# Optimization experiments

Hardware: AMD Instinct MI355X
Metric: run time of the kernel (lower is better)

## Reference

```python
import jax, jax.numpy as jnp
import numpy as np

EMB_DIM = 128
WEIGHT_COL = 24

def setup_inputs() -> dict:
    key = jax.random.key(0)
    ks = jax.random.split(key, 9)
    B, S = 8, 4096
    s_in = 1.0 / np.sqrt(EMB_DIM)
    s_out = 1.0 / np.sqrt(WEIGHT_COL)
    return {
        "x": jax.random.normal(ks[0], (B, S, EMB_DIM), dtype=jnp.float32),
        "wQ": jax.random.uniform(ks[1], (EMB_DIM, WEIGHT_COL), jnp.float32, -s_in, s_in),
        "bQ": jax.random.uniform(ks[2], (WEIGHT_COL,), jnp.float32, -s_in, s_in),
        "wK": jax.random.uniform(ks[3], (EMB_DIM, WEIGHT_COL), jnp.float32, -s_in, s_in),
        "bK": jax.random.uniform(ks[4], (WEIGHT_COL,), jnp.float32, -s_in, s_in),
        "wV": jax.random.uniform(ks[5], (EMB_DIM, WEIGHT_COL), jnp.float32, -s_in, s_in),
        "bV": jax.random.uniform(ks[6], (WEIGHT_COL,), jnp.float32, -s_in, s_in),
        "wO": jax.random.uniform(ks[7], (WEIGHT_COL, EMB_DIM), jnp.float32, -s_out, s_out),
        "bO": jax.random.uniform(ks[8], (EMB_DIM,), jnp.float32, -s_out, s_out),
    }

def reference(x, wQ, bQ, wK, bK, wV, bV, wO, bO):
    # projections: [B,S,E] -> [B,S,D]
    Q = x @ wQ + bQ
    K = x @ wK + bK
    V = x @ wV + bV
    # NOTE: source scales by sqrt(emb_dim), not sqrt(weight_col)
    scale = 1.0 / np.sqrt(EMB_DIM).astype(np.float32)
    scores = jnp.einsum('bqd,bkd->bqk', Q, K) * scale  # [B,S,S]
    A = jax.nn.softmax(scores, axis=-1)
    H = jnp.einsum('bqk,bkd->bqd', A, V)               # [B,S,D]
    return H @ wO + bO                                  # [B,S,E]
```

## Files before the change

kernel.cpp:

```cpp
#include <hip/hip_runtime.h>
#include <hip/hip_fp16.h>


#define B_ 8
#define S_ 4096
#define E_ 128
#define D_ 24
#define N_ (B_ * S_)
#define SCALE 0.08838834764831845f
#define LOG2E 1.4426950408889634f

#define NSP 8
#define KCHUNK (S_ / NSP)
#define TK 128

#define KS_STRIDE 40
#define VS_STRIDE 136
#define HS_STRIDE 40
#define XS_STRIDE 136
#define OS_STRIDE 84

typedef __attribute__((ext_vector_type(8))) short bfrag;
typedef __attribute__((ext_vector_type(4))) float ffrag;

__device__ inline unsigned short f2bf(float f) {
    unsigned int x = __builtin_bit_cast(unsigned int, f);
    return (unsigned short)((x + 0x7fffu + ((x >> 16) & 1u)) >> 16);
}
__device__ inline unsigned int pack2h(float a, float b) {
    unsigned int ua = __builtin_bit_cast(unsigned int, a) + 0x8000u;
    unsigned int ub = __builtin_bit_cast(unsigned int, b) + 0x8000u;
    return __builtin_amdgcn_perm(ub, ua, 0x07060302);
}
__device__ inline unsigned int packh16(float a, float b) {
    return __builtin_bit_cast(unsigned int, __builtin_amdgcn_cvt_pkrtz(a, b));
}

__global__ __launch_bounds__(256) void prep_kernel(
    const float* __restrict__ wQ, const float* __restrict__ bQ,
    const float* __restrict__ wK, const float* __restrict__ bK,
    const float* __restrict__ wV, const float* __restrict__ bV,
    const float* __restrict__ wO,
    unsigned short* __restrict__ Wf, unsigned short* __restrict__ wOf,
    float* __restrict__ bqkv)
{
    const int gtid   = blockIdx.x * 256 + threadIdx.x;
    const int stride = gridDim.x * 256;
    const float qs = SCALE * LOG2E;
    for (int idx = gtid; idx < 4 * 5 * 512; idx += stride) {
        const int j    = idx & 7;
        const int lane = (idx >> 3) & 63;
        const int nt   = (idx >> 9) % 5;
        const int kt   = idx / 2560;
        const int n = nt * 16 + (lane & 15);
        const int k = kt * 32 + ((lane >> 4) << 3) + j;
        float v = 0.0f;
        if (n < 24)      v = wQ[k * 24 + n] * qs;
        else if (n < 48) v = wK[k * 24 + (n - 24)];
        else if (n < 72) v = wV[k * 24 + (n - 48)];
        Wf[idx] = f2bf(v);
    }
    for (int idx = gtid; idx < 8 * 512; idx += stride) {
        const int j    = idx & 7;
        const int lane = (idx >> 3) & 63;
        const int nt   = idx >> 9;
        const int k = ((lane >> 4) << 3) + j;
        const int e = nt * 16 + (lane & 15);
        wOf[idx] = (k < 24) ? f2bf(wO[k * 128 + e]) : (unsigned short)0;
    }
    if (gtid < 80) {
        float v = 0.0f;
        if (gtid < 24)      v = bQ[gtid] * qs;
        else if (gtid < 48) v = bK[gtid - 24];
        else if (gtid < 72) v = bV[gtid - 48];
        bqkv[gtid] = v;
    }
}

__global__ __launch_bounds__(256) void proj_kernel(
    const float* __restrict__ x, const unsigned short* __restrict__ Wf,
    const float* __restrict__ bqkv,
    unsigned short* __restrict__ Qbf, unsigned short* __restrict__ Kbf,
    unsigned short* __restrict__ Vt)
{
    __shared__ float smem[64 * OS_STRIDE];
    unsigned short* xs = (unsigned short*)smem;
    float* os = smem;

    const int tid  = threadIdx.x;
    const int lane = tid & 63;
    const int w    = tid >> 6;
    const int col  = lane & 15;
    const int quad = lane >> 4;
    const int rb   = blockIdx.x * 64;

    #pragma unroll
    for (int i = 0; i < 8; ++i) {
        const int idx = i * 256 + tid;
        const int row = idx >> 5, c4 = idx & 31;
        const float4 xv = *(const float4*)(x + (size_t)(rb + row) * 128 + c4 * 4);
        uint2 h;
        h.x = pack2h(xv.x, xv.y);
        h.y = pack2h(xv.z, xv.w);
        *(uint2*)(&xs[row * XS_STRIDE + c4 * 4]) = h;
    }

    bfrag Wfr[20];
    #pragma unroll
    for (int f = 0; f < 20; ++f)
        Wfr[f] = *(const bfrag*)(Wf + (f * 64 + lane) * 8);

    __syncthreads();

    ffrag acc[5];
    #pragma unroll
    for (int nt = 0; nt < 5; ++nt) acc[nt] = (ffrag){0.f, 0.f, 0.f, 0.f};

    #pragma unroll
    for (int kt = 0; kt < 4; ++kt) {
        const bfrag Af = *(const bfrag*)(&xs[(w * 16 + col) * XS_STRIDE + kt * 32 + quad * 8]);
        #pragma unroll
        for (int nt = 0; nt < 5; ++nt)
            acc[nt] = __builtin_amdgcn_mfma_f32_16x16x32_bf16(Af, Wfr[kt * 5 + nt], acc[nt], 0, 0, 0);
    }

    __syncthreads();

    #pragma unroll
    for (int nt = 0; nt < 5; ++nt) {
        const float bb = bqkv[nt * 16 + col];
        #pragma unroll
        for (int r = 0; r < 4; ++r)
            os[(w * 16 + quad * 4 + r) * OS_STRIDE + nt * 16 + col] = acc[nt][r] + bb;
    }
    __syncthreads();

    {
        const int half  = tid & 1;
        const int row   = (tid >> 1) & 63;
        const int isK   = tid >> 7;
        const int cbase = isK * 24;
        unsigned int pk[8];
        #pragma unroll
        for (int g = 0; g < 8; ++g) {
            const int c0 = half * 16 + g * 2;
            const float f0 = (c0     < 24) ? os[row * OS_STRIDE + cbase + c0]     : 0.0f;
            const float f1 = (c0 + 1 < 24) ? os[row * OS_STRIDE + cbase + c0 + 1] : 0.0f;
            pk[g] = pack2h(f0, f1);
        }
        unsigned short* dst = (isK ? Kbf : Qbf) + (size_t)(rb + row) * 32 + half * 16;
        *(uint4*)(dst)     = make_uint4(pk[0], pk[1], pk[2], pk[3]);
        *(uint4*)(dst + 8) = make_uint4(pk[4], pk[5], pk[6], pk[7]);
    }

    if (tid < 192) {
        const int d  = tid % 24;
        const int ch = tid / 24;
        unsigned int p[4];
        #pragma unroll
        for (int g = 0; g < 4; ++g) {
            const float f0 = os[(ch * 8 + g * 2 + 0) * OS_STRIDE + 48 + d];
            const float f1 = os[(ch * 8 + g * 2 + 1) * OS_STRIDE + 48 + d];
            p[g] = pack2h(f0, f1);
        }
        const int b = rb >> 12, s0 = rb & 4095;
        uint4* dst = (uint4*)(Vt + (((size_t)(b * 32 + d)) << 12) + s0 + ch * 8);
        *dst = make_uint4(p[0], p[1], p[2], p[3]);
    } else if (tid < 200) {
        const int ch = tid - 192;
        const int b = rb >> 12, s0 = rb & 4095;
        uint4* dst = (uint4*)(Vt + (((size_t)(b * 32 + 24)) << 12) + s0 + ch * 8);
        *dst = make_uint4(0x3F803F80u, 0x3F803F80u, 0x3F803F80u, 0x3F803F80u);
    }
}

__global__ __launch_bounds__(256, 8) void attn_kernel(
    const unsigned short* __restrict__ Qbf, const unsigned short* __restrict__ Kbf,
    const unsigned short* __restrict__ Vt,
    __half* __restrict__ Opart, float* __restrict__ lpart)
{
    __shared__ unsigned short Ks[TK * KS_STRIDE];
    __shared__ unsigned short Vs[25 * VS_STRIDE];

    const int tid   = threadIdx.x;
    const int lane  = tid & 63;
    const int w     = tid >> 6;
    const int col   = lane & 15;
    const int quad  = lane >> 4;
    const int blk   = blockIdx.x;
    const int split = blockIdx.y;
    const int b     = blk >> 5;
    const int qbase = blk * 128 + w * 32;

    const bfrag Qf0 = *(const bfrag*)(Qbf + (size_t)(qbase + col) * 32 + quad * 8);
    const bfrag Qf1 = *(const bfrag*)(Qbf + (size_t)(qbase + 16 + col) * 32 + quad * 8);

    const unsigned short* Kbase = Kbf + ((size_t)b * 4096 + split * KCHUNK) * 32;
    const unsigned short* Vbase = Vt + (size_t)(b * 32) * 4096 + split * KCHUNK;

    const int r1 = (16 + col <= 24) ? (16 + col) : 24;

    ffrag O00 = {0.f,0.f,0.f,0.f};
    ffrag O01 = {0.f,0.f,0.f,0.f};
    ffrag O10 = {0.f,0.f,0.f,0.f};
    ffrag O11 = {0.f,0.f,0.f,0.f};

    for (int kb = 0; kb < KCHUNK; kb += TK) {
        #pragma unroll
        for (int i = 0; i < 2; ++i) {
            const int idx = i * 256 + tid;
            const int key = idx >> 2, ch = idx & 3;
            const uint4 t4 = *(const uint4*)(Kbase + (size_t)(kb + key) * 32 + ch * 8);
            const int row = (key & ~31) + (((key >> 2) & 1) << 4)
                          + (((key & 31) >> 3) << 2) + (key & 3);
            *(uint4*)(&Ks[row * KS_STRIDE + ch * 8]) = t4;
        }
        #pragma unroll
        for (int i = 0; i < 2; ++i) {
            const int idx = i * 256 + tid;
            if (idx < 400) {
                const int d = idx >> 4, ch = idx & 15;
                const uint4 t4 = *(const uint4*)(Vbase + (size_t)d * 4096 + kb + ch * 8);
                *(uint4*)(&Vs[d * VS_STRIDE + ch * 8]) = t4;
            }
        }
        __syncthreads();

        #pragma unroll
        for (int c2 = 0; c2 < 4; ++c2) {
            const bfrag Kfe = *(const bfrag*)(&Ks[(c2 * 32 + col) * KS_STRIDE + quad * 8]);
            const bfrag Kfo = *(const bfrag*)(&Ks[(c2 * 32 + 16 + col) * KS_STRIDE + quad * 8]);
            const bfrag Va0 = *(const bfrag*)(&Vs[col * VS_STRIDE + c2 * 32 + quad * 8]);
            const bfrag Va1 = *(const bfrag*)(&Vs[r1 * VS_STRIDE + c2 * 32 + quad * 8]);

            {
                ffrag Se = {0.f,0.f,0.f,0.f}, So = {0.f,0.f,0.f,0.f};
                Se = __builtin_amdgcn_mfma_f32_16x16x32_bf16(Kfe, Qf0, Se, 0, 0, 0);
                So = __builtin_amdgcn_mfma_f32_16x16x32_bf16(Kfo, Qf0, So, 0, 0, 0);
                union { bfrag f; unsigned int u[4]; } P;
                P.u[0] = pack2h(__builtin_amdgcn_exp2f(Se[0]), __builtin_amdgcn_exp2f(Se[1]));
                P.u[1] = pack2h(__builtin_amdgcn_exp2f(Se[2]), __builtin_amdgcn_exp2f(Se[3]));
                P.u[2] = pack2h(__builtin_amdgcn_exp2f(So[0]), __builtin_amdgcn_exp2f(So[1]));
                P.u[3] = pack2h(__builtin_amdgcn_exp2f(So[2]), __builtin_amdgcn_exp2f(So[3]));
                O00 = __builtin_amdgcn_mfma_f32_16x16x32_bf16(Va0, P.f, O00, 0, 0, 0);
                O01 = __builtin_amdgcn_mfma_f32_16x16x32_bf16(Va1, P.f, O01, 0, 0, 0);
            }
            {
                ffrag Se = {0.f,0.f,0.f,0.f}, So = {0.f,0.f,0.f,0.f};
                Se = __builtin_amdgcn_mfma_f32_16x16x32_bf16(Kfe, Qf1, Se, 0, 0, 0);
                So = __builtin_amdgcn_mfma_f32_16x16x32_bf16(Kfo, Qf1, So, 0, 0, 0);
                union { bfrag f; unsigned int u[4]; } P;
                P.u[0] = pack2h(__builtin_amdgcn_exp2f(Se[0]), __builtin_amdgcn_exp2f(Se[1]));
                P.u[1] = pack2h(__builtin_amdgcn_exp2f(Se[2]), __builtin_amdgcn_exp2f(Se[3]));
                P.u[2] = pack2h(__builtin_amdgcn_exp2f(So[0]), __builtin_amdgcn_exp2f(So[1]));
                P.u[3] = pack2h(__builtin_amdgcn_exp2f(So[2]), __builtin_amdgcn_exp2f(So[3]));
                O10 = __builtin_amdgcn_mfma_f32_16x16x32_bf16(Va0, P.f, O10, 0, 0, 0);
                O11 = __builtin_amdgcn_mfma_f32_16x16x32_bf16(Va1, P.f, O11, 0, 0, 0);
            }
        }
        __syncthreads();
    }

    {
        const size_t base0 = ((size_t)split * N_ + qbase + col) * 32;
        uint2 s0;
        s0.x = packh16(O00[0], O00[1]);
        s0.y = packh16(O00[2], O00[3]);
        *(uint2*)(Opart + base0 + quad * 4) = s0;
        if (quad < 2) {
            uint2 s1;
            s1.x = packh16(O01[0], O01[1]);
            s1.y = packh16(O01[2], O01[3]);
            *(uint2*)(Opart + base0 + 16 + quad * 4) = s1;
        }
        if (quad == 2)
            lpart[(size_t)split * N_ + qbase + col] = O01[0];

        const size_t base1 = base0 + 16 * 32;
        uint2 t0;
        t0.x = packh16(O10[0], O10[1]);
        t0.y = packh16(O10[2], O10[3]);
        *(uint2*)(Opart + base1 + quad * 4) = t0;
        if (quad < 2) {
            uint2 t1;
            t1.x = packh16(O11[0], O11[1]);
            t1.y = packh16(O11[2], O11[3]);
            *(uint2*)(Opart + base1 + 16 + quad * 4) = t1;
        }
        if (quad == 2)
            lpart[(size_t)split * N_ + qbase + 16 + col] = O11[0];
    }
}

__global__ __launch_bounds__(256) void combine_kernel(
    const __half* __restrict__ Opart, const float* __restrict__ lpart,
    const unsigned short* __restrict__ wOf, const float* __restrict__ bO,
    float* __restrict__ out)
{
    __shared__ unsigned short Hs[64 * HS_STRIDE];

    const int tid = threadIdx.x;
    const int qb  = blockIdx.x * 64;
    {
        const int ql = tid >> 2;
        const int c8 = (tid & 3) * 8;
        const int q  = qb + ql;
        float a[8] = {0.f, 0.f, 0.f, 0.f, 0.f, 0.f, 0.f, 0.f};
        if (c8 < 24) {
            #pragma unroll
            for (int s = 0; s < NSP; ++s) {
                const __half2* p2 = (const __half2*)(Opart + ((size_t)s * N_ + q) * 32 + c8);
                #pragma unroll
                for (int j = 0; j < 4; ++j) {
                    const float2 f = __half22float2(p2[j]);
                    a[2 * j]     += f.x;
                    a[2 * j + 1] += f.y;
                }
            }
        }
        float ls = 0.f;
        #pragma unroll
        for (int s = 0; s < NSP; ++s) ls += lpart[(size_t)s * N_ + q];
        const float inv = 1.0f / ls;
        uint4 pk;
        pk.x = pack2h(a[0] * inv, a[1] * inv);
        pk.y = pack2h(a[2] * inv, a[3] * inv);
        pk.z = pack2h(a[4] * inv, a[5] * inv);
        pk.w = pack2h(a[6] * inv, a[7] * inv);
        *(uint4*)(&Hs[ql * HS_STRIDE + c8]) = pk;
    }
    __syncthreads();

    const int lane = tid & 63;
    const int w    = tid >> 6;
    const int col  = lane & 15;
    const int quad = lane >> 4;
    const bfrag Hf = *(const bfrag*)(&Hs[(w * 16 + col) * HS_STRIDE + quad * 8]);
    #pragma unroll
    for (int nt = 0; nt < 8; ++nt) {
        const bfrag Wo = *(const bfrag*)(wOf + (nt * 64 + lane) * 8);
        ffrag C = {0.f, 0.f, 0.f, 0.f};
        C = __builtin_amdgcn_mfma_f32_16x16x32_bf16(Hf, Wo, C, 0, 0, 0);
        const float bo = bO[nt * 16 + col];
        #pragma unroll
        for (int r = 0; r < 4; ++r)
            out[(size_t)(qb + w * 16 + quad * 4 + r) * 128 + nt * 16 + col] = C[r] + bo;
    }
}

extern "C" void kernel_launch(void* const* d_in, const int* in_sizes, int n_in,
                              void* d_out, int out_size, void* d_ws, size_t ws_size,
                              hipStream_t stream) {
    const float* x  = (const float*)d_in[0];
    const float* wQ = (const float*)d_in[1];
    const float* bQ = (const float*)d_in[2];
    const float* wK = (const float*)d_in[3];
    const float* bK = (const float*)d_in[4];
    const float* wV = (const float*)d_in[5];
    const float* bV = (const float*)d_in[6];
    const float* wO = (const float*)d_in[7];
    const float* bO = (const float*)d_in[8];
    float* out = (float*)d_out;

    unsigned short* ws16 = (unsigned short*)d_ws;
    unsigned short* Qbf = ws16;
    unsigned short* Kbf = Qbf + (size_t)N_ * 32;
    unsigned short* Vt  = Kbf + (size_t)N_ * 32;
    unsigned short* Wf  = Vt + (size_t)B_ * 32 * S_;
    unsigned short* wOf = Wf + 4 * 5 * 512;
    float* bqkv = (float*)(wOf + 8 * 512);
    __half* Opart = (__half*)(bqkv + 80);
    float* lpart = (float*)(Opart + (size_t)NSP * N_ * 32);

    prep_kernel<<<8, 256, 0, stream>>>(wQ, bQ, wK, bK, wV, bV, wO, Wf, wOf, bqkv);
    proj_kernel<<<N_ / 64, 256, 0, stream>>>(x, Wf, bqkv, Qbf, Kbf, Vt);
    attn_kernel<<<dim3(N_ / 128, NSP), 256, 0, stream>>>(Qbf, Kbf, Vt, Opart, lpart);
    combine_kernel<<<N_ / 64, 256, 0, stream>>>(Opart, lpart, wOf, bO, out);
}
```

Measured before the change: 125.4 us.

## Double-buffer K/V tiles with register prefetch and larger attention blocks

The attention kernel now prefetches the next K/V tile from global memory into registers while it computes on the current tile from a double-buffered shared memory region. This removes one barrier per iteration and hides global load latency. Blocks grow to 512 threads covering 256 queries, and the key-split count drops from 8 to 4. That halves the partial outputs the combine kernel has to read, but leaves fewer blocks and longer per-block loops, and the larger LDS footprint lowers occupancy.

```diff
diff --git a/kernel.cpp b/kernel.cpp
--- a/kernel.cpp
+++ b/kernel.cpp
@@ -10,9 +10,10 @@
 #define SCALE 0.08838834764831845f
 #define LOG2E 1.4426950408889634f
 
-#define NSP 8
+#define NSP 4
 #define KCHUNK (S_ / NSP)
 #define TK 128
+#define NT (KCHUNK / TK)
 
 #define KS_STRIDE 40
 #define VS_STRIDE 136
@@ -174,13 +175,13 @@
     }
 }
 
-__global__ __launch_bounds__(256, 8) void attn_kernel(
+__global__ __launch_bounds__(512, 4) void attn_kernel(
     const unsigned short* __restrict__ Qbf, const unsigned short* __restrict__ Kbf,
     const unsigned short* __restrict__ Vt,
     __half* __restrict__ Opart, float* __restrict__ lpart)
 {
-    __shared__ unsigned short Ks[TK * KS_STRIDE];
-    __shared__ unsigned short Vs[25 * VS_STRIDE];
+    __shared__ unsigned short Ks[2 * TK * KS_STRIDE];
+    __shared__ unsigned short Vs[2 * 25 * VS_STRIDE];
 
     const int tid   = threadIdx.x;
     const int lane  = tid & 63;
@@ -189,14 +190,19 @@
     const int quad  = lane >> 4;
     const int blk   = blockIdx.x;
     const int split = blockIdx.y;
-    const int b     = blk >> 5;
-    const int qbase = blk * 128 + w * 32;
+    const int b     = blk >> 4;
+    const int qbase = blk * 256 + w * 32;
 
     const bfrag Qf0 = *(const bfrag*)(Qbf + (size_t)(qbase + col) * 32 + quad * 8);
     const bfrag Qf1 = *(const bfrag*)(Qbf + (size_t)(qbase + 16 + col) * 32 + quad * 8);
 
     const unsigned short* Kbase = Kbf + ((size_t)b * 4096 + split * KCHUNK) * 32;
     const unsigned short* Vbase = Vt + (size_t)(b * 32) * 4096 + split * KCHUNK;
+
+    const int skey = tid >> 2, sch = tid & 3;
+    const int srow = (skey & ~31) + (((skey >> 2) & 1) << 4)
+                   + (((skey & 31) >> 3) << 2) + (skey & 3);
+    const int sd = tid >> 4, svch = tid & 15;
 
     const int r1 = (16 + col <= 24) ? (16 + col) : 24;
 
@@ -205,33 +211,13 @@
     ffrag O10 = {0.f,0.f,0.f,0.f};
     ffrag O11 = {0.f,0.f,0.f,0.f};
 
-    for (int kb = 0; kb < KCHUNK; kb += TK) {
-        #pragma unroll
-        for (int i = 0; i < 2; ++i) {
-            const int idx = i * 256 + tid;
-            const int key = idx >> 2, ch = idx & 3;
-            const uint4 t4 = *(const uint4*)(Kbase + (size_t)(kb + key) * 32 + ch * 8);
-            const int row = (key & ~31) + (((key >> 2) & 1) << 4)
-                          + (((key & 31) >> 3) << 2) + (key & 3);
-            *(uint4*)(&Ks[row * KS_STRIDE + ch * 8]) = t4;
-        }
-        #pragma unroll
-        for (int i = 0; i < 2; ++i) {
-            const int idx = i * 256 + tid;
-            if (idx < 400) {
-                const int d = idx >> 4, ch = idx & 15;
-                const uint4 t4 = *(const uint4*)(Vbase + (size_t)d * 4096 + kb + ch * 8);
-                *(uint4*)(&Vs[d * VS_STRIDE + ch * 8]) = t4;
-            }
-        }
-        __syncthreads();
-
+    auto compute_tile = [&](const unsigned short* ksb, const unsigned short* vsb) {
         #pragma unroll
         for (int c2 = 0; c2 < 4; ++c2) {
-            const bfrag Kfe = *(const bfrag*)(&Ks[(c2 * 32 + col) * KS_STRIDE + quad * 8]);
-            const bfrag Kfo = *(const bfrag*)(&Ks[(c2 * 32 + 16 + col) * KS_STRIDE + quad * 8]);
-            const bfrag Va0 = *(const bfrag*)(&Vs[col * VS_STRIDE + c2 * 32 + quad * 8]);
-            const bfrag Va1 = *(const bfrag*)(&Vs[r1 * VS_STRIDE + c2 * 32 + quad * 8]);
+            const bfrag Kfe = *(const bfrag*)(&ksb[(c2 * 32 + col) * KS_STRIDE + quad * 8]);
+            const bfrag Kfo = *(const bfrag*)(&ksb[(c2 * 32 + 16 + col) * KS_STRIDE + quad * 8]);
+            const bfrag Va0 = *(const bfrag*)(&vsb[col * VS_STRIDE + c2 * 32 + quad * 8]);
+            const bfrag Va1 = *(const bfrag*)(&vsb[r1 * VS_STRIDE + c2 * 32 + quad * 8]);
 
             {
                 ffrag Se = {0.f,0.f,0.f,0.f}, So = {0.f,0.f,0.f,0.f};
@@ -258,8 +244,37 @@
                 O11 = __builtin_amdgcn_mfma_f32_16x16x32_bf16(Va1, P.f, O11, 0, 0, 0);
             }
         }
+    };
+
+    {
+        const uint4 k4 = *(const uint4*)(Kbase + (size_t)skey * 32 + sch * 8);
+        *(uint4*)(&Ks[srow * KS_STRIDE + sch * 8]) = k4;
+        if (tid < 400) {
+            const uint4 v4 = *(const uint4*)(Vbase + (size_t)sd * 4096 + svch * 8);
+            *(uint4*)(&Vs[sd * VS_STRIDE + svch * 8]) = v4;
+        }
+    }
+    __syncthreads();
+
+    int cur = 0;
+    for (int t = 0; t < NT - 1; ++t) {
+        const int kb = (t + 1) * TK;
+        const uint4 k4 = *(const uint4*)(Kbase + (size_t)(kb + skey) * 32 + sch * 8);
+        uint4 v4;
+        if (tid < 400)
+            v4 = *(const uint4*)(Vbase + (size_t)sd * 4096 + kb + svch * 8);
+        __builtin_amdgcn_sched_barrier(0);
+
+        compute_tile(Ks + cur * (TK * KS_STRIDE), Vs + cur * (25 * VS_STRIDE));
+
+        const int nxt = cur ^ 1;
+        *(uint4*)(&Ks[nxt * (TK * KS_STRIDE) + srow * KS_STRIDE + sch * 8]) = k4;
+        if (tid < 400)
+            *(uint4*)(&Vs[nxt * (25 * VS_STRIDE) + sd * VS_STRIDE + svch * 8]) = v4;
         __syncthreads();
-    }
+        cur = nxt;
+    }
+    compute_tile(Ks + cur * (TK * KS_STRIDE), Vs + cur * (25 * VS_STRIDE));
 
     {
         const size_t base0 = ((size_t)split * N_ + qbase + col) * 32;
@@ -374,6 +389,6 @@
 
     prep_kernel<<<8, 256, 0, stream>>>(wQ, bQ, wK, bK, wV, bV, wO, Wf, wOf, bqkv);
     proj_kernel<<<N_ / 64, 256, 0, stream>>>(x, Wf, bqkv, Qbf, Kbf, Vt);
-    attn_kernel<<<dim3(N_ / 128, NSP), 256, 0, stream>>>(Qbf, Kbf, Vt, Opart, lpart);
+    attn_kernel<<<dim3(N_ / 256, NSP), 512, 0, stream>>>(Qbf, Kbf, Vt, Opart, lpart);
     combine_kernel<<<N_ / 64, 256, 0, stream>>>(Opart, lpart, wOf, bO, out);
 }
```

Measured after the change: 119.3 us. 1.05x faster.
